# Performance work log

Measured on AMD Instinct MI355X. Metric: run time of the kernel, lower is better.

Reference implementation:

```python
import jax, jax.numpy as jnp
import numpy as np

PENALTY_MATRIX = jnp.array([[0.0, 1.0, 2.0],
                            [5.0, 0.0, 1.0],
                            [20.0, 10.0, 0.0]], dtype=jnp.float32)
CRITICAL_MISS_PENALTY = 20.0


def setup_inputs() -> dict:
    key = jax.random.key(0)
    k1, k2 = jax.random.split(key)
    B, C = 4194304, 3
    outputs = jax.random.normal(k1, (B, C), dtype=jnp.float32)
    targets = jax.random.randint(k2, (B,), 0, C, dtype=jnp.int64)
    return {"outputs": outputs, "targets": targets}


def reference(outputs, targets):
    # Cross-entropy (mean over batch, no class weights)
    logp = jax.nn.log_softmax(outputs, axis=-1)              # [B, 3]
    ce_loss = -jnp.mean(jnp.take_along_axis(logp, targets[:, None].astype(jnp.int32), axis=-1))

    pred = jnp.argmax(outputs, axis=-1)                      # [B]

    # Vectorized penalty-matrix gather replaces per-sample python loop
    safety_penalty = jnp.mean(PENALTY_MATRIX[targets, pred])

    # Critical-miss penalty (class 2)
    critical_mask = targets == 2
    n_crit = jnp.sum(critical_mask).astype(jnp.float32)
    misses = jnp.sum(critical_mask & (pred != 2)).astype(jnp.float32)
    critical_penalty = jnp.where(n_crit > 0, misses / jnp.maximum(n_crit, 1.0) * CRITICAL_MISS_PENALTY, 0.0)

    return ce_loss + 0.3 * safety_penalty + 0.5 * critical_penalty
```

## Files before the change

### kernel.cpp

```cpp
#include <hip/hip_runtime.h>


__device__ __forceinline__ float wave_reduce_f(float v) {
#pragma unroll
    for (int off = 32; off > 0; off >>= 1) v += __shfl_down(v, off, 64);
    return v;
}
__device__ __forceinline__ double wave_reduce_d(double v) {
#pragma unroll
    for (int off = 32; off > 0; off >>= 1) v += __shfl_down(v, off, 64);
    return v;
}

__device__ __forceinline__ void process_quad(const float4 a, const float4 b,
                                             const float4 c, const int4 t4,
                                             float& ce, float& pen,
                                             int& crit, int& miss) {
    const float x[12] = {a.x, a.y, a.z, a.w, b.x, b.y, b.z, b.w, c.x, c.y, c.z, c.w};
    const int   t[4]  = {t4.x, t4.y, t4.z, t4.w};
#pragma unroll
    for (int s = 0; s < 4; ++s) {
        const float x0 = x[3 * s + 0], x1 = x[3 * s + 1], x2 = x[3 * s + 2];
        const int tg = t[s];

        int pred = 0;
        float best = x0;
        if (x1 > best) { best = x1; pred = 1; }
        if (x2 > best) { best = x2; pred = 2; }

        const float e0 = __expf(x0 - best);
        const float e1 = __expf(x1 - best);
        const float e2 = __expf(x2 - best);
        const float lse = best + __logf(e0 + e1 + e2);
        const float xt = (tg == 0) ? x0 : ((tg == 1) ? x1 : x2);
        ce += (lse - xt);

        float pv;
        if (tg == 0)      pv = (float)pred;
        else if (tg == 1) pv = (pred == 0) ? 5.0f : ((pred == 1) ? 0.0f : 1.0f);
        else              pv = (pred == 0) ? 20.0f : ((pred == 1) ? 10.0f : 0.0f);
        pen += pv;

        const int is_crit = (tg == 2);
        crit += is_crit;
        miss += is_crit & (pred != 2);
    }
}

__global__ void __launch_bounds__(256) loss_main_kernel(
    const float* __restrict__ logits, const int* __restrict__ tgt,
    int nquads, float4* __restrict__ partials) {
    float ce = 0.0f, pen = 0.0f;
    int crit = 0, miss = 0;

    const float4* lv = reinterpret_cast<const float4*>(logits);
    const int4*   tv = reinterpret_cast<const int4*>(tgt);

    const int stride = gridDim.x * blockDim.x;
    for (int q = blockIdx.x * blockDim.x + threadIdx.x; q < nquads; q += stride) {
        const float4 a = lv[3 * q + 0];
        const float4 b = lv[3 * q + 1];
        const float4 c = lv[3 * q + 2];
        const int4   t4 = tv[q];
        process_quad(a, b, c, t4, ce, pen, crit, miss);
    }

    ce = wave_reduce_f(ce);
    pen = wave_reduce_f(pen);
    float fcrit = wave_reduce_f((float)crit);
    float fmiss = wave_reduce_f((float)miss);

    __shared__ float4 s_part[4];
    const int lane = threadIdx.x & 63;
    const int wid  = threadIdx.x >> 6;
    if (lane == 0) s_part[wid] = make_float4(ce, pen, fcrit, fmiss);
    __syncthreads();
    if (threadIdx.x == 0) {
        float4 r = s_part[0];
#pragma unroll
        for (int i = 1; i < 4; ++i) {
            r.x += s_part[i].x; r.y += s_part[i].y;
            r.z += s_part[i].z; r.w += s_part[i].w;
        }
        partials[blockIdx.x] = r;
    }
}

__global__ void __launch_bounds__(256) loss_final_kernel(
    const float4* __restrict__ partials, int nblocks,
    const float* __restrict__ logits, const int* __restrict__ tgt,
    int start, int total, float* __restrict__ out) {
    double ce = 0.0, pen = 0.0, cr = 0.0, mi = 0.0;
    for (int i = threadIdx.x; i < nblocks; i += 256) {
        const float4 p = partials[i];
        ce += (double)p.x; pen += (double)p.y;
        cr += (double)p.z; mi += (double)p.w;
    }
    ce = wave_reduce_d(ce); pen = wave_reduce_d(pen);
    cr = wave_reduce_d(cr); mi = wave_reduce_d(mi);

    __shared__ double sd[4][4];
    const int lane = threadIdx.x & 63;
    const int wid  = threadIdx.x >> 6;
    if (lane == 0) { sd[wid][0] = ce; sd[wid][1] = pen; sd[wid][2] = cr; sd[wid][3] = mi; }
    __syncthreads();
    if (threadIdx.x == 0) {
#pragma unroll
        for (int i = 1; i < 4; ++i) {
            sd[0][0] += sd[i][0]; sd[0][1] += sd[i][1];
            sd[0][2] += sd[i][2]; sd[0][3] += sd[i][3];
        }
        ce = sd[0][0]; pen = sd[0][1]; cr = sd[0][2]; mi = sd[0][3];

        for (int i = start; i < total; ++i) {
            const float x0 = logits[3 * i + 0], x1 = logits[3 * i + 1], x2 = logits[3 * i + 2];
            const int tg = tgt[i];
            int pred = 0;
            float best = x0;
            if (x1 > best) { best = x1; pred = 1; }
            if (x2 > best) { best = x2; pred = 2; }
            const float e0 = __expf(x0 - best), e1 = __expf(x1 - best), e2 = __expf(x2 - best);
            const float lse = best + __logf(e0 + e1 + e2);
            const float xt = (tg == 0) ? x0 : ((tg == 1) ? x1 : x2);
            ce += (double)(lse - xt);
            float pv;
            if (tg == 0)      pv = (float)pred;
            else if (tg == 1) pv = (pred == 0) ? 5.0f : ((pred == 1) ? 0.0f : 1.0f);
            else              pv = (pred == 0) ? 20.0f : ((pred == 1) ? 10.0f : 0.0f);
            pen += (double)pv;
            cr += (double)(tg == 2);
            mi += (double)((tg == 2) && (pred != 2));
        }

        const double inv_b = 1.0 / (double)total;
        const double ce_loss = ce * inv_b;
        const double safety  = pen * inv_b;
        const double crit_pen = (cr > 0.0) ? (mi / cr * 20.0) : 0.0;
        out[0] = (float)(ce_loss + 0.3 * safety + 0.5 * crit_pen);
    }
}

extern "C" void kernel_launch(void* const* d_in, const int* in_sizes, int n_in,
                              void* d_out, int out_size, void* d_ws, size_t ws_size,
                              hipStream_t stream) {
    const float* logits = (const float*)d_in[0];
    const int*   tgt    = (const int*)d_in[1];
    const int B = in_sizes[1];

    float4* partials = (float4*)d_ws;

    const int nquads = B / 4;
    int blocks = 2048;
    const int needed = (nquads + 255) / 256;
    if (blocks > needed) blocks = needed;
    const int maxp = (int)(ws_size / sizeof(float4));
    if (blocks > maxp) blocks = maxp;
    if (blocks < 1) blocks = 1;

    loss_main_kernel<<<blocks, 256, 0, stream>>>(logits, tgt, nquads, partials);
    loss_final_kernel<<<1, 256, 0, stream>>>(partials, blocks, logits, tgt,
                                             nquads * 4, B, (float*)d_out);
}
```

Measured before the change: 21.11 us.

## Stage logits through swizzled LDS for fully coalesced global loads

Each block now processes 1024-sample chunks. The logits are loaded cooperatively as contiguous float4s, so consecutive threads read consecutive addresses, and stored into shared memory with an XOR swizzle to avoid bank conflicts. Each thread then reads back its own three float4s. The aim is to replace the stride-3 float4 global access pattern with perfectly coalesced loads. The cost is two barriers per chunk and extra LDS traffic, which may reduce memory-level parallelism.

```diff
diff --git a/kernel.cpp b/kernel.cpp
--- a/kernel.cpp
+++ b/kernel.cpp
@@ -47,22 +47,35 @@
     }
 }
 
+__device__ __forceinline__ int swz(int g) { return g ^ ((g >> 3) & 7); }
+
 __global__ void __launch_bounds__(256) loss_main_kernel(
     const float* __restrict__ logits, const int* __restrict__ tgt,
-    int nquads, float4* __restrict__ partials) {
+    int nchunks, float4* __restrict__ partials) {
     float ce = 0.0f, pen = 0.0f;
     int crit = 0, miss = 0;
 
     const float4* lv = reinterpret_cast<const float4*>(logits);
     const int4*   tv = reinterpret_cast<const int4*>(tgt);
 
-    const int stride = gridDim.x * blockDim.x;
-    for (int q = blockIdx.x * blockDim.x + threadIdx.x; q < nquads; q += stride) {
-        const float4 a = lv[3 * q + 0];
-        const float4 b = lv[3 * q + 1];
-        const float4 c = lv[3 * q + 2];
-        const int4   t4 = tv[q];
+    __shared__ float4 s_f4[768];
+
+    for (int chunk = blockIdx.x; chunk < nchunks; chunk += gridDim.x) {
+        const float4* src = lv + (size_t)chunk * 768;
+#pragma unroll
+        for (int s = 0; s < 3; ++s) {
+            const int g = threadIdx.x + 256 * s;
+            s_f4[swz(g)] = src[g];
+        }
+        const int4 t4 = tv[(size_t)chunk * 256 + threadIdx.x];
+        __syncthreads();
+
+        const int g0 = 3 * threadIdx.x;
+        const float4 a = s_f4[swz(g0 + 0)];
+        const float4 b = s_f4[swz(g0 + 1)];
+        const float4 c = s_f4[swz(g0 + 2)];
         process_quad(a, b, c, t4, ce, pen, crit, miss);
+        __syncthreads();
     }
 
     ce = wave_reduce_f(ce);
@@ -149,15 +162,14 @@
 
     float4* partials = (float4*)d_ws;
 
-    const int nquads = B / 4;
+    const int nchunks = B / 1024;
     int blocks = 2048;
-    const int needed = (nquads + 255) / 256;
-    if (blocks > needed) blocks = needed;
+    if (blocks > nchunks) blocks = nchunks;
     const int maxp = (int)(ws_size / sizeof(float4));
     if (blocks > maxp) blocks = maxp;
     if (blocks < 1) blocks = 1;
 
-    loss_main_kernel<<<blocks, 256, 0, stream>>>(logits, tgt, nquads, partials);
+    loss_main_kernel<<<blocks, 256, 0, stream>>>(logits, tgt, nchunks, partials);
     loss_final_kernel<<<1, 256, 0, stream>>>(partials, blocks, logits, tgt,
-                                             nquads * 4, B, (float*)d_out);
+                                             nchunks * 1024, B, (float*)d_out);
 }
```

New measurement: 20.95 us. Within noise of the previous version (-0.8%).

## Fuse final reduction into main kernel via last-block atomic ticket

Applied to the files above, without the earlier changes.

Merges the two-kernel reduction into one kernel. Each block writes its partial and takes an atomic ticket, and the last block to finish reduces all partials and writes the loss. This drops the second kernel launch and its gap, but adds a memset of the ticket counter on the stream, a threadfence and an atomic per block, and a serial tail in one block.

```diff
diff --git a/kernel.cpp b/kernel.cpp
--- a/kernel.cpp
+++ b/kernel.cpp
@@ -47,17 +47,19 @@
     }
 }
 
-__global__ void __launch_bounds__(256) loss_main_kernel(
+__global__ void __launch_bounds__(256) loss_fused_kernel(
     const float* __restrict__ logits, const int* __restrict__ tgt,
-    int nquads, float4* __restrict__ partials) {
+    int nquads, int total,
+    unsigned int* __restrict__ ticket, float4* __restrict__ partials,
+    float* __restrict__ out) {
     float ce = 0.0f, pen = 0.0f;
     int crit = 0, miss = 0;
 
     const float4* lv = reinterpret_cast<const float4*>(logits);
     const int4*   tv = reinterpret_cast<const int4*>(tgt);
 
-    const int stride = gridDim.x * blockDim.x;
-    for (int q = blockIdx.x * blockDim.x + threadIdx.x; q < nquads; q += stride) {
+    const int nthreads = gridDim.x * blockDim.x;
+    for (int q = blockIdx.x * blockDim.x + threadIdx.x; q < nquads; q += nthreads) {
         const float4 a = lv[3 * q + 0];
         const float4 b = lv[3 * q + 1];
         const float4 c = lv[3 * q + 2];
@@ -71,6 +73,7 @@
     float fmiss = wave_reduce_f((float)miss);
 
     __shared__ float4 s_part[4];
+    __shared__ bool s_last;
     const int lane = threadIdx.x & 63;
     const int wid  = threadIdx.x >> 6;
     if (lane == 0) s_part[wid] = make_float4(ce, pen, fcrit, fmiss);
@@ -83,26 +86,25 @@
             r.z += s_part[i].z; r.w += s_part[i].w;
         }
         partials[blockIdx.x] = r;
+        __threadfence();
+        const unsigned int t = atomicAdd(ticket, 1u);
+        s_last = (t == gridDim.x - 1);
     }
-}
+    __syncthreads();
+    if (!s_last) return;
 
-__global__ void __launch_bounds__(256) loss_final_kernel(
-    const float4* __restrict__ partials, int nblocks,
-    const float* __restrict__ logits, const int* __restrict__ tgt,
-    int start, int total, float* __restrict__ out) {
-    double ce = 0.0, pen = 0.0, cr = 0.0, mi = 0.0;
-    for (int i = threadIdx.x; i < nblocks; i += 256) {
+    __threadfence();
+    double dce = 0.0, dpen = 0.0, dcr = 0.0, dmi = 0.0;
+    for (int i = threadIdx.x; i < (int)gridDim.x; i += blockDim.x) {
         const float4 p = partials[i];
-        ce += (double)p.x; pen += (double)p.y;
-        cr += (double)p.z; mi += (double)p.w;
+        dce += (double)p.x; dpen += (double)p.y;
+        dcr += (double)p.z; dmi += (double)p.w;
     }
-    ce = wave_reduce_d(ce); pen = wave_reduce_d(pen);
-    cr = wave_reduce_d(cr); mi = wave_reduce_d(mi);
+    dce = wave_reduce_d(dce); dpen = wave_reduce_d(dpen);
+    dcr = wave_reduce_d(dcr); dmi = wave_reduce_d(dmi);
 
     __shared__ double sd[4][4];
-    const int lane = threadIdx.x & 63;
-    const int wid  = threadIdx.x >> 6;
-    if (lane == 0) { sd[wid][0] = ce; sd[wid][1] = pen; sd[wid][2] = cr; sd[wid][3] = mi; }
+    if (lane == 0) { sd[wid][0] = dce; sd[wid][1] = dpen; sd[wid][2] = dcr; sd[wid][3] = dmi; }
     __syncthreads();
     if (threadIdx.x == 0) {
 #pragma unroll
@@ -110,9 +112,9 @@
             sd[0][0] += sd[i][0]; sd[0][1] += sd[i][1];
             sd[0][2] += sd[i][2]; sd[0][3] += sd[i][3];
         }
-        ce = sd[0][0]; pen = sd[0][1]; cr = sd[0][2]; mi = sd[0][3];
+        dce = sd[0][0]; dpen = sd[0][1]; dcr = sd[0][2]; dmi = sd[0][3];
 
-        for (int i = start; i < total; ++i) {
+        for (int i = nquads * 4; i < total; ++i) {
             const float x0 = logits[3 * i + 0], x1 = logits[3 * i + 1], x2 = logits[3 * i + 2];
             const int tg = tgt[i];
             int pred = 0;
@@ -122,20 +124,20 @@
             const float e0 = __expf(x0 - best), e1 = __expf(x1 - best), e2 = __expf(x2 - best);
             const float lse = best + __logf(e0 + e1 + e2);
             const float xt = (tg == 0) ? x0 : ((tg == 1) ? x1 : x2);
-            ce += (double)(lse - xt);
+            dce += (double)(lse - xt);
             float pv;
             if (tg == 0)      pv = (float)pred;
             else if (tg == 1) pv = (pred == 0) ? 5.0f : ((pred == 1) ? 0.0f : 1.0f);
             else              pv = (pred == 0) ? 20.0f : ((pred == 1) ? 10.0f : 0.0f);
-            pen += (double)pv;
-            cr += (double)(tg == 2);
-            mi += (double)((tg == 2) && (pred != 2));
+            dpen += (double)pv;
+            dcr += (double)(tg == 2);
+            dmi += (double)((tg == 2) && (pred != 2));
         }
 
         const double inv_b = 1.0 / (double)total;
-        const double ce_loss = ce * inv_b;
-        const double safety  = pen * inv_b;
-        const double crit_pen = (cr > 0.0) ? (mi / cr * 20.0) : 0.0;
+        const double ce_loss = dce * inv_b;
+        const double safety  = dpen * inv_b;
+        const double crit_pen = (dcr > 0.0) ? (dmi / dcr * 20.0) : 0.0;
         out[0] = (float)(ce_loss + 0.3 * safety + 0.5 * crit_pen);
     }
 }
@@ -147,17 +149,19 @@
     const int*   tgt    = (const int*)d_in[1];
     const int B = in_sizes[1];
 
-    float4* partials = (float4*)d_ws;
+    unsigned int* ticket   = (unsigned int*)d_ws;
+    float4*       partials = (float4*)((char*)d_ws + 256);
 
     const int nquads = B / 4;
     int blocks = 2048;
     const int needed = (nquads + 255) / 256;
     if (blocks > needed) blocks = needed;
-    const int maxp = (int)(ws_size / sizeof(float4));
+    const int maxp = (int)((ws_size - 256) / sizeof(float4));
     if (blocks > maxp) blocks = maxp;
     if (blocks < 1) blocks = 1;
 
-    loss_main_kernel<<<blocks, 256, 0, stream>>>(logits, tgt, nquads, partials);
-    loss_final_kernel<<<1, 256, 0, stream>>>(partials, blocks, logits, tgt,
-                                             nquads * 4, B, (float*)d_out);
+    hipMemsetAsync(d_ws, 0, 4, stream);
+
+    loss_fused_kernel<<<blocks, 256, 0, stream>>>(logits, tgt, nquads, B,
+                                                  ticket, partials, (float*)d_out);
 }
```

Result: slower. 81.46 us (+285.8%).
